# Optimization experiments

Measured on AMD Instinct MI355X. Metric: run time of the kernel, lower is better.

## Reference

```python
import jax, jax.numpy as jnp
import numpy as np

B, S, K, V = 512, 1024, 128, 512
SCALE = float(np.sqrt(K))


def setup_inputs() -> dict:
    key0 = jax.random.key(0)
    ks = jax.random.split(key0, 16)
    inp = {
        "keys": jax.random.normal(ks[0], (B, S, K), jnp.float32),
        "values": jax.random.normal(ks[1], (B, S, V), jnp.float32),
        "key": jax.random.normal(ks[2], (B, K), jnp.float32),
        "value": jax.random.normal(ks[3], (B, V), jnp.float32),
        "hidden": jax.random.normal(ks[4], (B, V), jnp.float32),
        "write_ptr": jax.random.randint(ks[5], (B,), 0, S, jnp.int64).astype(jnp.int64),
        "filled": jax.random.randint(ks[6], (B,), 0, S, jnp.int64).astype(jnp.int64),
        # parameters (Linear: y = x @ W.T + b)
        "Wq": jax.random.normal(ks[7], (K, V), jnp.float32) / np.sqrt(V),
        "bq": jnp.zeros((K,), jnp.float32),
        "Wg1": jax.random.normal(ks[8], (V, 2 * V), jnp.float32) / np.sqrt(2 * V),
        "bg1": jnp.zeros((V,), jnp.float32),
        "Wg2": jax.random.normal(ks[9], (V, V), jnp.float32) / np.sqrt(V),
        "bg2": jnp.zeros((V,), jnp.float32),
        "Wo": jax.random.normal(ks[10], (V, V), jnp.float32) / np.sqrt(V),
        "bo": jnp.zeros((V,), jnp.float32),
    }
    return inp


def reference(keys, values, key, value, hidden, write_ptr, filled,
              Wq, bq, Wg1, bg1, Wg2, bg2, Wo, bo):
    b_idx = jnp.arange(B)
    # --- write (ring-buffer scatter; torch does it under no_grad) ---
    keys_w = keys.at[b_idx, write_ptr].set(jax.lax.stop_gradient(key))
    values_w = values.at[b_idx, write_ptr].set(jax.lax.stop_gradient(value))
    filled_w = jnp.minimum(filled + 1, S)
    # --- read ---
    query = hidden @ Wq.T + bq                                  # (B, K)
    scores = jnp.einsum('bsk,bk->bs', keys_w, query) / SCALE     # (B, S)
    valid = jnp.arange(S)[None, :] < filled_w[:, None]           # (B, S)
    scores = jnp.where(valid, scores, -jnp.inf)
    attn = jax.nn.softmax(scores, axis=-1)
    attn = jnp.nan_to_num(attn, nan=0.0)
    retrieved = jnp.einsum('bs,bsv->bv', attn, values_w)         # (B, V)
    h_cat = jnp.concatenate([hidden, retrieved], axis=-1)        # (B, 2V)
    g = jax.nn.silu(h_cat @ Wg1.T + bg1)
    gate = jax.nn.sigmoid(g @ Wg2.T + bg2)
    out = (hidden + gate * retrieved) @ Wo.T + bo                # (B, V)
    return out
```

## Files before the change

### kernel.cpp

```cpp
#include <hip/hip_runtime.h>
#include <math.h>

#define BB 512
#define SS 1024
#define KK 128
#define VV 512
#define NC 16
#define CH 64
#define KS 8

static constexpr float INV_SCALE = 0.088388347648318447f;

__global__ __launch_bounds__(128) void q_kernel(
    const float* __restrict__ hidden, const float* __restrict__ Wq,
    const float* __restrict__ bq, float* __restrict__ qout)
{
    __shared__ __align__(16) float hid[VV];
    const int b = blockIdx.x, t = threadIdx.x;
    ((float4*)hid)[t] = ((const float4*)(hidden + (size_t)b * VV))[t];
    __syncthreads();
    const float4* w4 = (const float4*)(Wq + (size_t)t * VV);
    const float4* h4 = (const float4*)hid;
    float acc = 0.f;
    #pragma unroll 8
    for (int v = 0; v < VV / 4; ++v) {
        float4 a = w4[v], h = h4[v];
        acc += a.x * h.x + a.y * h.y + a.z * h.z + a.w * h.w;
    }
    qout[(size_t)b * KK + t] = acc + bq[t];
}

__global__ __launch_bounds__(256) void attn_chunk_kernel(
    const float* __restrict__ keys, const float* __restrict__ values,
    const float* __restrict__ keyv, const float* __restrict__ valv,
    const float* __restrict__ q,
    const int* __restrict__ write_ptr, const int* __restrict__ filled,
    float* __restrict__ ml, float* __restrict__ accp)
{
    __shared__ __align__(16) float qs[KK];
    __shared__ __align__(16) float p[CH];
    __shared__ __align__(16) float red[4];
    __shared__ __align__(16) float4 pvp[VV / 4];

    const int bc = blockIdx.x;
    const int b = bc >> 4;
    const int c = bc & 15;
    const int t = threadIdx.x;
    const int wave = t >> 6, lane = t & 63;

    int f = filled[b] + 1; if (f > SS) f = SS;
    const int sbeg = c * CH;
    int n = f - sbeg; if (n > CH) n = CH;

    float* mlrow = ml + ((size_t)b * NC + c) * 2;
    float* arow  = accp + ((size_t)b * NC + c) * VV;

    if (n <= 0) {
        if (t == 0) { mlrow[0] = -INFINITY; mlrow[1] = 0.f; }
        return;
    }

    if (t < KK / 4) ((float4*)qs)[t] = ((const float4*)(q + (size_t)b * KK))[t];
    __syncthreads();

    const int sub = lane & 31, rsel = lane >> 5;
    const int srow = wave * 2 + rsel;
    const float4 q4 = ((const float4*)qs)[sub];
    const float* kb = keys + ((size_t)b * SS + sbeg) * KK;
    const float* kw = keyv + (size_t)b * KK;
    const int wpl = write_ptr[b] - sbeg;

    const int nmain = n & ~31;
    for (int s0 = 0; s0 < nmain; s0 += 32) {
        float4 kv[4];
        #pragma unroll
        for (int u = 0; u < 4; ++u) {
            const int s = s0 + u * 8 + srow;
            const float* kr = (s == wpl) ? kw : (kb + (size_t)s * KK);
            kv[u] = ((const float4*)kr)[sub];
        }
        #pragma unroll
        for (int u = 0; u < 4; ++u) {
            float prt = kv[u].x * q4.x + kv[u].y * q4.y
                      + kv[u].z * q4.z + kv[u].w * q4.w;
            prt += __shfl_xor(prt, 16);
            prt += __shfl_xor(prt, 8);
            prt += __shfl_xor(prt, 4);
            prt += __shfl_xor(prt, 2);
            prt += __shfl_xor(prt, 1);
            if (sub == 0) p[s0 + u * 8 + srow] = prt * INV_SCALE;
        }
    }
    for (int s = nmain + srow; s < n; s += 8) {
        const float* kr = (s == wpl) ? kw : (kb + (size_t)s * KK);
        const float4 kv = ((const float4*)kr)[sub];
        float prt = kv.x * q4.x + kv.y * q4.y + kv.z * q4.z + kv.w * q4.w;
        prt += __shfl_xor(prt, 16);
        prt += __shfl_xor(prt, 8);
        prt += __shfl_xor(prt, 4);
        prt += __shfl_xor(prt, 2);
        prt += __shfl_xor(prt, 1);
        if (sub == 0) p[s] = prt * INV_SCALE;
    }
    __syncthreads();

    float lmax = -INFINITY;
    for (int i = t; i < n; i += 256) lmax = fmaxf(lmax, p[i]);
    lmax = fmaxf(lmax, __shfl_xor(lmax, 32));
    lmax = fmaxf(lmax, __shfl_xor(lmax, 16));
    lmax = fmaxf(lmax, __shfl_xor(lmax, 8));
    lmax = fmaxf(lmax, __shfl_xor(lmax, 4));
    lmax = fmaxf(lmax, __shfl_xor(lmax, 2));
    lmax = fmaxf(lmax, __shfl_xor(lmax, 1));
    if (lane == 0) red[wave] = lmax;
    __syncthreads();
    const float m = fmaxf(fmaxf(red[0], red[1]), fmaxf(red[2], red[3]));
    float lsum = 0.f;
    for (int i = t; i < n; i += 256) {
        const float e = __expf(p[i] - m);
        p[i] = e;
        lsum += e;
    }
    lsum += __shfl_xor(lsum, 32);
    lsum += __shfl_xor(lsum, 16);
    lsum += __shfl_xor(lsum, 8);
    lsum += __shfl_xor(lsum, 4);
    lsum += __shfl_xor(lsum, 2);
    lsum += __shfl_xor(lsum, 1);
    __syncthreads();
    if (lane == 0) red[wave] = lsum;
    __syncthreads();
    const float l = red[0] + red[1] + red[2] + red[3];

    const int col4 = t & 127, stream = t >> 7;
    const float4* vb = (const float4*)(values + ((size_t)b * SS + sbeg) * VV);
    const float4* vw = (const float4*)(valv + (size_t)b * VV);
    float4 acc = make_float4(0.f, 0.f, 0.f, 0.f);
    const int nm2 = n & ~15;
    for (int s0 = 0; s0 < nm2; s0 += 16) {
        float4 v[8]; float ps[8];
        #pragma unroll
        for (int u = 0; u < 8; ++u) {
            const int s = s0 + u * 2 + stream;
            const float4* vr = (s == wpl) ? vw : (vb + (size_t)s * (VV / 4));
            v[u] = vr[col4];
            ps[u] = p[s];
        }
        #pragma unroll
        for (int u = 0; u < 8; ++u) {
            acc.x += ps[u] * v[u].x;
            acc.y += ps[u] * v[u].y;
            acc.z += ps[u] * v[u].z;
            acc.w += ps[u] * v[u].w;
        }
    }
    for (int s = nm2 + stream; s < n; s += 2) {
        const float4* vr = (s == wpl) ? vw : (vb + (size_t)s * (VV / 4));
        const float4 v = vr[col4];
        const float psv = p[s];
        acc.x += psv * v.x;
        acc.y += psv * v.y;
        acc.z += psv * v.z;
        acc.w += psv * v.w;
    }
    if (stream == 1) pvp[col4] = acc;
    __syncthreads();
    if (stream == 0) {
        const float4 o = pvp[col4];
        ((float4*)arow)[col4] = make_float4(acc.x + o.x, acc.y + o.y,
                                            acc.z + o.z, acc.w + o.w);
    }
    if (t == 0) { mlrow[0] = m; mlrow[1] = l; }
}

__global__ __launch_bounds__(128) void combine_kernel(
    const float* __restrict__ hidden, const float* __restrict__ ml,
    const float* __restrict__ accp, float* __restrict__ hcat)
{
    const int b = blockIdx.x, t = threadIdx.x;
    const float* mlb = ml + (size_t)b * NC * 2;
    float mv[NC], lv[NC];
    #pragma unroll
    for (int c = 0; c < NC; ++c) { mv[c] = mlb[2 * c]; lv[c] = mlb[2 * c + 1]; }
    float ms = mv[0];
    #pragma unroll
    for (int c = 1; c < NC; ++c) ms = fmaxf(ms, mv[c]);
    float w[NC], denom = 0.f;
    #pragma unroll
    for (int c = 0; c < NC; ++c) { w[c] = __expf(mv[c] - ms); denom += w[c] * lv[c]; }
    const float invd = 1.f / denom;
    float4 r = make_float4(0.f, 0.f, 0.f, 0.f);
    for (int c = 0; c < NC; ++c) {
        if (lv[c] != 0.f) {
            const float4 x = ((const float4*)(accp + ((size_t)b * NC + c) * VV))[t];
            r.x += w[c] * x.x; r.y += w[c] * x.y;
            r.z += w[c] * x.z; r.w += w[c] * x.w;
        }
    }
    r.x *= invd; r.y *= invd; r.z *= invd; r.w *= invd;
    float4* hc = (float4*)(hcat + (size_t)b * 2 * VV);
    hc[t] = ((const float4*)(hidden + (size_t)b * VV))[t];
    hc[VV / 4 + t] = r;
}

__global__ __launch_bounds__(256) void gemm_ks_kernel(
    const float* __restrict__ A, int K, const float* __restrict__ W,
    float* __restrict__ part)
{
    __shared__ __align__(16) float As[16][68];
    __shared__ __align__(16) float Bs[16][68];
    const int bx = blockIdx.x;
    const int mt = bx & 7, nt = (bx >> 3) & 7, ks = bx >> 6;
    const int kseg = K >> 3;
    const int kbeg = ks * kseg, kend = kbeg + kseg;
    const int t = threadIdx.x;
    const int tx = t & 15, ty = t >> 4;
    const int m0 = mt << 6, n0 = nt << 6;
    const int ra = t >> 2, ca = (t & 3) << 2;
    float4 a0 = {0,0,0,0}, a1 = {0,0,0,0}, a2 = {0,0,0,0}, a3 = {0,0,0,0};

    for (int k0 = kbeg; k0 < kend; k0 += 16) {
        const float4 av = *(const float4*)(A + (size_t)(m0 + ra) * K + k0 + ca);
        const float4 wv = *(const float4*)(W + (size_t)(n0 + ra) * K + k0 + ca);
        As[ca + 0][ra] = av.x;
        As[ca + 1][ra] = av.y;
        As[ca + 2][ra] = av.z;
        As[ca + 3][ra] = av.w;
        Bs[ca + 0][ra] = wv.x;
        Bs[ca + 1][ra] = wv.y;
        Bs[ca + 2][ra] = wv.z;
        Bs[ca + 3][ra] = wv.w;
        __syncthreads();
        #pragma unroll
        for (int k = 0; k < 16; ++k) {
            const float4 a = *(const float4*)&As[k][ty << 2];
            const float4 b = *(const float4*)&Bs[k][tx << 2];
            a0.x += a.x * b.x; a0.y += a.x * b.y; a0.z += a.x * b.z; a0.w += a.x * b.w;
            a1.x += a.y * b.x; a1.y += a.y * b.y; a1.z += a.y * b.z; a1.w += a.y * b.w;
            a2.x += a.z * b.x; a2.y += a.z * b.y; a2.z += a.z * b.z; a2.w += a.z * b.w;
            a3.x += a.w * b.x; a3.y += a.w * b.y; a3.z += a.w * b.z; a3.w += a.w * b.w;
        }
        __syncthreads();
    }
    float* pp = part + ((size_t)(ks * 512 + m0 + (ty << 2))) * 512 + n0 + (tx << 2);
    *(float4*)(pp + 0 * 512) = a0;
    *(float4*)(pp + 1 * 512) = a1;
    *(float4*)(pp + 2 * 512) = a2;
    *(float4*)(pp + 3 * 512) = a3;
}

__global__ __launch_bounds__(128) void reduce_silu_kernel(
    const float* __restrict__ part, const float* __restrict__ bg1,
    float* __restrict__ G)
{
    const int b = blockIdx.x, t = threadIdx.x;
    const size_t o = (size_t)b * (VV / 4) + t;
    const size_t st = (size_t)512 * (VV / 4);
    const float4* p4 = (const float4*)part;
    const float4 bb = ((const float4*)bg1)[t];
    float4 s = bb;
    #pragma unroll
    for (int k = 0; k < KS; ++k) {
        const float4 pv = p4[o + (size_t)k * st];
        s.x += pv.x; s.y += pv.y; s.z += pv.z; s.w += pv.w;
    }
    float4 g;
    g.x = s.x / (1.f + __expf(-s.x));
    g.y = s.y / (1.f + __expf(-s.y));
    g.z = s.z / (1.f + __expf(-s.z));
    g.w = s.w / (1.f + __expf(-s.w));
    ((float4*)G)[o] = g;
}

__global__ __launch_bounds__(128) void reduce_gate_kernel(
    const float* __restrict__ part, const float* __restrict__ bg2,
    const float* __restrict__ hcat, float* __restrict__ X)
{
    const int b = blockIdx.x, t = threadIdx.x;
    const size_t o = (size_t)b * (VV / 4) + t;
    const size_t st = (size_t)512 * (VV / 4);
    const float4* p4 = (const float4*)part;
    const float4 bb = ((const float4*)bg2)[t];
    float4 s = bb;
    #pragma unroll
    for (int k = 0; k < KS; ++k) {
        const float4 pv = p4[o + (size_t)k * st];
        s.x += pv.x; s.y += pv.y; s.z += pv.z; s.w += pv.w;
    }
    const float4* hc = (const float4*)(hcat + (size_t)b * 2 * VV);
    const float4 h = hc[t];
    const float4 r = hc[VV / 4 + t];
    float4 x;
    x.x = h.x + r.x / (1.f + __expf(-s.x));
    x.y = h.y + r.y / (1.f + __expf(-s.y));
    x.z = h.z + r.z / (1.f + __expf(-s.z));
    x.w = h.w + r.w / (1.f + __expf(-s.w));
    ((float4*)X)[o] = x;
}

__global__ __launch_bounds__(128) void reduce_bias_kernel(
    const float* __restrict__ part, const float* __restrict__ bo,
    float* __restrict__ out)
{
    const int b = blockIdx.x, t = threadIdx.x;
    const size_t o = (size_t)b * (VV / 4) + t;
    const size_t st = (size_t)512 * (VV / 4);
    const float4* p4 = (const float4*)part;
    const float4 bb = ((const float4*)bo)[t];
    float4 s = bb;
    #pragma unroll
    for (int k = 0; k < KS; ++k) {
        const float4 pv = p4[o + (size_t)k * st];
        s.x += pv.x; s.y += pv.y; s.z += pv.z; s.w += pv.w;
    }
    ((float4*)out)[o] = s;
}

extern "C" void kernel_launch(void* const* d_in, const int* in_sizes, int n_in,
                              void* d_out, int out_size, void* d_ws, size_t ws_size,
                              hipStream_t stream) {
    const float* keys    = (const float*)d_in[0];
    const float* values  = (const float*)d_in[1];
    const float* keyv    = (const float*)d_in[2];
    const float* valv    = (const float*)d_in[3];
    const float* hidden  = (const float*)d_in[4];
    const int*   wptr    = (const int*)d_in[5];
    const int*   filled  = (const int*)d_in[6];
    const float* Wq  = (const float*)d_in[7];
    const float* bq  = (const float*)d_in[8];
    const float* Wg1 = (const float*)d_in[9];
    const float* bg1 = (const float*)d_in[10];
    const float* Wg2 = (const float*)d_in[11];
    const float* bg2 = (const float*)d_in[12];
    const float* Wo  = (const float*)d_in[13];
    const float* bo  = (const float*)d_in[14];
    float* out = (float*)d_out;

    float* ws   = (float*)d_ws;
    float* q    = ws;
    float* ml   = q + (size_t)BB * KK;
    float* accp = ml + (size_t)BB * NC * 2;
    float* hcat = accp + (size_t)BB * NC * VV;
    float* G    = hcat + (size_t)BB * 2 * VV;
    float* X    = G + (size_t)BB * VV;
    float* part = X + (size_t)BB * VV;

    q_kernel<<<BB, 128, 0, stream>>>(hidden, Wq, bq, q);
    attn_chunk_kernel<<<BB * NC, 256, 0, stream>>>(keys, values, keyv, valv, q,
                                                   wptr, filled, ml, accp);
    combine_kernel<<<BB, 128, 0, stream>>>(hidden, ml, accp, hcat);

    gemm_ks_kernel<<<64 * KS, 256, 0, stream>>>(hcat, 2 * VV, Wg1, part);
    reduce_silu_kernel<<<BB, 128, 0, stream>>>(part, bg1, G);

    gemm_ks_kernel<<<64 * KS, 256, 0, stream>>>(G, VV, Wg2, part);
    reduce_gate_kernel<<<BB, 128, 0, stream>>>(part, bg2, hcat, X);

    gemm_ks_kernel<<<64 * KS, 256, 0, stream>>>(X, VV, Wo, part);
    reduce_bias_kernel<<<BB, 128, 0, stream>>>(part, bo, out);
}
```

Measured before the change: 221.1 us.

## Fuse split-K reductions into next GEMM loads, batch q projection, nontemporal KV loads

Removes the separate reduce_silu and reduce_gate kernels by having each following GEMM sum the split-K partials, add the bias and apply the activation while it loads its A tile. Split-K drops from 8 to 4 segments. The q projection now handles 8 batch rows per block and stages Wq in shared memory, so each weight row is read fewer times. Keys and values are read with nontemporal loads to keep the streaming data out of cache. In exchange, the fused GEMMs recompute the partial sums and activations once per N tile, and partial buffers get their own workspace regions.

```diff
diff --git a/kernel.cpp b/kernel.cpp
--- a/kernel.cpp
+++ b/kernel.cpp
@@ -7,27 +7,63 @@
 #define VV 512
 #define NC 16
 #define CH 64
-#define KS 8
+#define KS 4
+#define QB 8
 
 static constexpr float INV_SCALE = 0.088388347648318447f;
 
-__global__ __launch_bounds__(128) void q_kernel(
+typedef float nfloat4 __attribute__((ext_vector_type(4)));
+
+__device__ __forceinline__ float4 ntload(const float4* p) {
+    nfloat4 v = __builtin_nontemporal_load((const nfloat4*)p);
+    return make_float4(v.x, v.y, v.z, v.w);
+}
+
+__global__ __launch_bounds__(256) void q_kernel(
     const float* __restrict__ hidden, const float* __restrict__ Wq,
     const float* __restrict__ bq, float* __restrict__ qout)
 {
-    __shared__ __align__(16) float hid[VV];
-    const int b = blockIdx.x, t = threadIdx.x;
-    ((float4*)hid)[t] = ((const float4*)(hidden + (size_t)b * VV))[t];
-    __syncthreads();
-    const float4* w4 = (const float4*)(Wq + (size_t)t * VV);
-    const float4* h4 = (const float4*)hid;
-    float acc = 0.f;
-    #pragma unroll 8
-    for (int v = 0; v < VV / 4; ++v) {
-        float4 a = w4[v], h = h4[v];
-        acc += a.x * h.x + a.y * h.y + a.z * h.z + a.w * h.w;
-    }
-    qout[(size_t)b * KK + t] = acc + bq[t];
+    __shared__ float hidb[QB][516];
+    __shared__ float wqt[16][516];
+    __shared__ float qp[16][QB][2];
+    const int blk = blockIdx.x;
+    const int t = threadIdx.x;
+    const int b0 = blk * QB;
+
+    for (int i = t; i < QB * 128; i += 256) {
+        const int bl = i >> 7, c4 = i & 127;
+        *(float4*)&hidb[bl][c4 * 4] =
+            ((const float4*)(hidden + (size_t)(b0 + bl) * VV))[c4];
+    }
+    for (int k0 = 0; k0 < KK; k0 += 16) {
+        __syncthreads();
+        for (int i = t; i < 16 * 128; i += 256) {
+            const int kl = i >> 7, c4 = i & 127;
+            *(float4*)&wqt[kl][c4 * 4] =
+                ((const float4*)(Wq + (size_t)(k0 + kl) * VV))[c4];
+        }
+        __syncthreads();
+        {
+            const int p = t & 127, half = t >> 7;
+            const int kl = p >> 3, bl = p & 7;
+            const float* wr = &wqt[kl][half * 256];
+            const float* hr = &hidb[bl][half * 256];
+            float acc = 0.f;
+            #pragma unroll
+            for (int j = 0; j < 64; ++j) {
+                const float4 wv = *(const float4*)&wr[j * 4];
+                const float4 hv = *(const float4*)&hr[j * 4];
+                acc += wv.x * hv.x + wv.y * hv.y + wv.z * hv.z + wv.w * hv.w;
+            }
+            qp[kl][bl][half] = acc;
+        }
+        __syncthreads();
+        if (t < 128) {
+            const int kl = t >> 3, bl = t & 7;
+            qout[(size_t)(b0 + bl) * KK + k0 + kl] =
+                qp[kl][bl][0] + qp[kl][bl][1] + bq[k0 + kl];
+        }
+    }
 }
 
 __global__ __launch_bounds__(256) void attn_chunk_kernel(
@@ -77,7 +113,7 @@
         for (int u = 0; u < 4; ++u) {
             const int s = s0 + u * 8 + srow;
             const float* kr = (s == wpl) ? kw : (kb + (size_t)s * KK);
-            kv[u] = ((const float4*)kr)[sub];
+            kv[u] = ntload(((const float4*)kr) + sub);
         }
         #pragma unroll
         for (int u = 0; u < 4; ++u) {
@@ -93,7 +129,7 @@
     }
     for (int s = nmain + srow; s < n; s += 8) {
         const float* kr = (s == wpl) ? kw : (kb + (size_t)s * KK);
-        const float4 kv = ((const float4*)kr)[sub];
+        const float4 kv = ntload(((const float4*)kr) + sub);
         float prt = kv.x * q4.x + kv.y * q4.y + kv.z * q4.z + kv.w * q4.w;
         prt += __shfl_xor(prt, 16);
         prt += __shfl_xor(prt, 8);
@@ -143,7 +179,7 @@
         for (int u = 0; u < 8; ++u) {
             const int s = s0 + u * 2 + stream;
             const float4* vr = (s == wpl) ? vw : (vb + (size_t)s * (VV / 4));
-            v[u] = vr[col4];
+            v[u] = ntload(vr + col4);
             ps[u] = p[s];
         }
         #pragma unroll
@@ -156,7 +192,7 @@
     }
     for (int s = nm2 + stream; s < n; s += 2) {
         const float4* vr = (s == wpl) ? vw : (vb + (size_t)s * (VV / 4));
-        const float4 v = vr[col4];
+        const float4 v = ntload(vr + col4);
         const float psv = p[s];
         acc.x += psv * v.x;
         acc.y += psv * v.y;
@@ -204,23 +240,49 @@
 }
 
 __global__ __launch_bounds__(256) void gemm_ks_kernel(
-    const float* __restrict__ A, int K, const float* __restrict__ W,
-    float* __restrict__ part)
+    const float* __restrict__ Agl, int K, const float* __restrict__ W,
+    const float* __restrict__ prev, const float* __restrict__ bias,
+    const float* __restrict__ hc, float* __restrict__ part, int mode)
 {
     __shared__ __align__(16) float As[16][68];
     __shared__ __align__(16) float Bs[16][68];
     const int bx = blockIdx.x;
     const int mt = bx & 7, nt = (bx >> 3) & 7, ks = bx >> 6;
-    const int kseg = K >> 3;
+    const int kseg = K >> 2;
     const int kbeg = ks * kseg, kend = kbeg + kseg;
     const int t = threadIdx.x;
     const int tx = t & 15, ty = t >> 4;
     const int m0 = mt << 6, n0 = nt << 6;
     const int ra = t >> 2, ca = (t & 3) << 2;
+    const size_t pst = (size_t)VV * VV;
     float4 a0 = {0,0,0,0}, a1 = {0,0,0,0}, a2 = {0,0,0,0}, a3 = {0,0,0,0};
 
     for (int k0 = kbeg; k0 < kend; k0 += 16) {
-        const float4 av = *(const float4*)(A + (size_t)(m0 + ra) * K + k0 + ca);
+        float4 av;
+        if (mode == 0) {
+            av = *(const float4*)(Agl + (size_t)(m0 + ra) * K + k0 + ca);
+        } else {
+            const size_t off = (size_t)(m0 + ra) * VV + k0 + ca;
+            float4 s = *(const float4*)(bias + k0 + ca);
+            #pragma unroll
+            for (int sx = 0; sx < KS; ++sx) {
+                const float4 pv = *(const float4*)(prev + (size_t)sx * pst + off);
+                s.x += pv.x; s.y += pv.y; s.z += pv.z; s.w += pv.w;
+            }
+            if (mode == 1) {
+                av.x = s.x / (1.f + __expf(-s.x));
+                av.y = s.y / (1.f + __expf(-s.y));
+                av.z = s.z / (1.f + __expf(-s.z));
+                av.w = s.w / (1.f + __expf(-s.w));
+            } else {
+                const float4 h  = *(const float4*)(hc + (size_t)(m0 + ra) * (2 * VV) + k0 + ca);
+                const float4 rr = *(const float4*)(hc + (size_t)(m0 + ra) * (2 * VV) + VV + k0 + ca);
+                av.x = h.x + rr.x / (1.f + __expf(-s.x));
+                av.y = h.y + rr.y / (1.f + __expf(-s.y));
+                av.z = h.z + rr.z / (1.f + __expf(-s.z));
+                av.w = h.w + rr.w / (1.f + __expf(-s.w));
+            }
+        }
         const float4 wv = *(const float4*)(W + (size_t)(n0 + ra) * K + k0 + ca);
         As[ca + 0][ra] = av.x;
         As[ca + 1][ra] = av.y;
@@ -242,60 +304,12 @@
         }
         __syncthreads();
     }
-    float* pp = part + ((size_t)(ks * 512 + m0 + (ty << 2))) * 512 + n0 + (tx << 2);
-    *(float4*)(pp + 0 * 512) = a0;
-    *(float4*)(pp + 1 * 512) = a1;
-    *(float4*)(pp + 2 * 512) = a2;
-    *(float4*)(pp + 3 * 512) = a3;
-}
-
-__global__ __launch_bounds__(128) void reduce_silu_kernel(
-    const float* __restrict__ part, const float* __restrict__ bg1,
-    float* __restrict__ G)
-{
-    const int b = blockIdx.x, t = threadIdx.x;
-    const size_t o = (size_t)b * (VV / 4) + t;
-    const size_t st = (size_t)512 * (VV / 4);
-    const float4* p4 = (const float4*)part;
-    const float4 bb = ((const float4*)bg1)[t];
-    float4 s = bb;
-    #pragma unroll
-    for (int k = 0; k < KS; ++k) {
-        const float4 pv = p4[o + (size_t)k * st];
-        s.x += pv.x; s.y += pv.y; s.z += pv.z; s.w += pv.w;
-    }
-    float4 g;
-    g.x = s.x / (1.f + __expf(-s.x));
-    g.y = s.y / (1.f + __expf(-s.y));
-    g.z = s.z / (1.f + __expf(-s.z));
-    g.w = s.w / (1.f + __expf(-s.w));
-    ((float4*)G)[o] = g;
-}
-
-__global__ __launch_bounds__(128) void reduce_gate_kernel(
-    const float* __restrict__ part, const float* __restrict__ bg2,
-    const float* __restrict__ hcat, float* __restrict__ X)
-{
-    const int b = blockIdx.x, t = threadIdx.x;
-    const size_t o = (size_t)b * (VV / 4) + t;
-    const size_t st = (size_t)512 * (VV / 4);
-    const float4* p4 = (const float4*)part;
-    const float4 bb = ((const float4*)bg2)[t];
-    float4 s = bb;
-    #pragma unroll
-    for (int k = 0; k < KS; ++k) {
-        const float4 pv = p4[o + (size_t)k * st];
-        s.x += pv.x; s.y += pv.y; s.z += pv.z; s.w += pv.w;
-    }
-    const float4* hc = (const float4*)(hcat + (size_t)b * 2 * VV);
-    const float4 h = hc[t];
-    const float4 r = hc[VV / 4 + t];
-    float4 x;
-    x.x = h.x + r.x / (1.f + __expf(-s.x));
-    x.y = h.y + r.y / (1.f + __expf(-s.y));
-    x.z = h.z + r.z / (1.f + __expf(-s.z));
-    x.w = h.w + r.w / (1.f + __expf(-s.w));
-    ((float4*)X)[o] = x;
+    float* pp = part + (size_t)ks * pst
+              + (size_t)(m0 + (ty << 2)) * VV + n0 + (tx << 2);
+    *(float4*)(pp + 0 * VV) = a0;
+    *(float4*)(pp + 1 * VV) = a1;
+    *(float4*)(pp + 2 * VV) = a2;
+    *(float4*)(pp + 3 * VV) = a3;
 }
 
 __global__ __launch_bounds__(128) void reduce_bias_kernel(
@@ -304,7 +318,7 @@
 {
     const int b = blockIdx.x, t = threadIdx.x;
     const size_t o = (size_t)b * (VV / 4) + t;
-    const size_t st = (size_t)512 * (VV / 4);
+    const size_t st = (size_t)VV * (VV / 4);
     const float4* p4 = (const float4*)part;
     const float4 bb = ((const float4*)bo)[t];
     float4 s = bb;
@@ -336,26 +350,28 @@
     const float* bo  = (const float*)d_in[14];
     float* out = (float*)d_out;
 
-    float* ws   = (float*)d_ws;
-    float* q    = ws;
-    float* ml   = q + (size_t)BB * KK;
-    float* accp = ml + (size_t)BB * NC * 2;
-    float* hcat = accp + (size_t)BB * NC * VV;
-    float* G    = hcat + (size_t)BB * 2 * VV;
-    float* X    = G + (size_t)BB * VV;
-    float* part = X + (size_t)BB * VV;
-
-    q_kernel<<<BB, 128, 0, stream>>>(hidden, Wq, bq, q);
+    float* ws    = (float*)d_ws;
+    float* q     = ws;
+    float* ml    = q + (size_t)BB * KK;
+    float* accp  = ml + (size_t)BB * NC * 2;
+    float* hcat  = accp + (size_t)BB * NC * VV;
+    float* part1 = hcat + (size_t)BB * 2 * VV;
+    float* part2 = part1 + (size_t)KS * VV * VV;
+    float* part3 = part2 + (size_t)KS * VV * VV;
+
+    q_kernel<<<BB / QB, 256, 0, stream>>>(hidden, Wq, bq, q);
     attn_chunk_kernel<<<BB * NC, 256, 0, stream>>>(keys, values, keyv, valv, q,
                                                    wptr, filled, ml, accp);
     combine_kernel<<<BB, 128, 0, stream>>>(hidden, ml, accp, hcat);
 
-    gemm_ks_kernel<<<64 * KS, 256, 0, stream>>>(hcat, 2 * VV, Wg1, part);
-    reduce_silu_kernel<<<BB, 128, 0, stream>>>(part, bg1, G);
-
-    gemm_ks_kernel<<<64 * KS, 256, 0, stream>>>(G, VV, Wg2, part);
-    reduce_gate_kernel<<<BB, 128, 0, stream>>>(part, bg2, hcat, X);
-
-    gemm_ks_kernel<<<64 * KS, 256, 0, stream>>>(X, VV, Wo, part);
-    reduce_bias_kernel<<<BB, 128, 0, stream>>>(part, bo, out);
-}
+    gemm_ks_kernel<<<64 * KS, 256, 0, stream>>>(hcat, 2 * VV, Wg1,
+                                                nullptr, nullptr, nullptr,
+                                                part1, 0);
+    gemm_ks_kernel<<<64 * KS, 256, 0, stream>>>(nullptr, VV, Wg2,
+                                                part1, bg1, nullptr,
+                                                part2, 1);
+    gemm_ks_kernel<<<64 * KS, 256, 0, stream>>>(nullptr, VV, Wo,
+                                                part2, bg2, hcat,
+                                                part3, 2);
+    reduce_bias_kernel<<<BB, 128, 0, stream>>>(part3, bo, out);
+}
```

Result: faster. 211.2 us (-4.5%).
